# Kernel tuning notes

Hardware: AMD Instinct MI355X
Metric: run time of the kernel (lower is better)

The kernel has to match this reference:

```python
import jax, jax.numpy as jnp
import numpy as np

ALPHA = 0.2  # LeakyReLU negative slope

def setup_inputs() -> dict:
    key = jax.random.key(0)
    k1, k2 = jax.random.split(key)
    K, N = 4096, 1024
    x = jax.random.normal(k1, (K, N), dtype=jnp.float32)
    # xavier_uniform with gain 1.414 on shape (2N, 1)
    limit = 1.414 * np.sqrt(6.0 / (2 * N + 1))
    w = jax.random.uniform(k2, (2 * N, 1), dtype=jnp.float32, minval=-limit, maxval=limit)
    return {"x": x, "w": w}

def reference(x, w):
    # Faithful to: e[i,j] = leakyrelu(concat(x[i], x[j]) @ w)
    # Split w into halves -> outer-sum score (same math, no KxK x 2N intermediate).
    N = x.shape[1]
    w1 = w[:N, 0]   # (N,)
    w2 = w[N:, 0]   # (N,)
    s1 = x @ w1     # (K,)
    s2 = x @ w2     # (K,)
    e = jax.nn.leaky_relu(s1[:, None] + s2[None, :], negative_slope=ALPHA)  # (K, K)
    attention = jax.nn.softmax(e, axis=1)  # dropout p=0.0 -> identity
    h = attention @ x  # (K, N)
    return h
```

## Files before the change

kernel.cpp:

```cpp
#include <hip/hip_runtime.h>

#define KDIM 4096
#define NDIM 1024
#define ALPHA 0.2f
#define LOG2E 1.4426950408889634f
#define CCH 256
#define RCH 16
#define PFL 256

__device__ __align__(16) float g_s1L[KDIM];
__device__ __align__(16) float g_s2L[KDIM];
__device__ __align__(16) float g_E [2 * KDIM];
__device__ __align__(16) float g_F1[KDIM];
__device__ __align__(16) float g_F2[KDIM];
__device__ __align__(16) int   g_t  [KDIM];
__device__ __align__(16) int   g_sig[KDIM];
__device__ __align__(16) float g_cs [CCH][2 * NDIM];
__device__ __align__(16) float g_pre[CCH][2 * NDIM];
__device__ __align__(16) float g_tot[2 * NDIM];
__device__ __align__(16) float g_cz [2 * CCH];
__device__ __align__(16) float g_zpre[2 * CCH];
__device__ __align__(16) float g_ztot[2];

__global__ __launch_bounds__(256) void k_dots(const float* __restrict__ x,
                                              const float* __restrict__ w){
  const int wid = threadIdx.x >> 6, lane = threadIdx.x & 63;
  const int row = blockIdx.x * 4 + wid;
  const float* xr = x + (size_t)row * NDIM;
  float d1 = 0.f, d2 = 0.f;
  #pragma unroll
  for (int q = 0; q < 4; ++q){
    const int off = q * 256 + lane * 4;
    float4 X  = *(const float4*)(xr + off);
    float4 W1 = *(const float4*)(w + off);
    float4 W2 = *(const float4*)(w + NDIM + off);
    d1 = fmaf(X.x, W1.x, fmaf(X.y, W1.y, fmaf(X.z, W1.z, fmaf(X.w, W1.w, d1))));
    d2 = fmaf(X.x, W2.x, fmaf(X.y, W2.y, fmaf(X.z, W2.z, fmaf(X.w, W2.w, d2))));
  }
  #pragma unroll
  for (int m = 32; m >= 1; m >>= 1){
    d1 += __shfl_xor(d1, m, 64);
    d2 += __shfl_xor(d2, m, 64);
  }
  if (lane == 0){
    const float s1 = d1 * LOG2E, s2 = d2 * LOG2E;
    g_s1L[row] = s1;
    g_s2L[row] = s2;
    g_E[2 * row]     = __builtin_amdgcn_exp2f(s2);
    g_E[2 * row + 1] = __builtin_amdgcn_exp2f(ALPHA * s2);
    g_F1[row] = __builtin_amdgcn_exp2f(s1);
    g_F2[row] = __builtin_amdgcn_exp2f(ALPHA * s1);
  }
}

__global__ __launch_bounds__(256) void k_rank(){
  __shared__ __align__(16) float s2s[KDIM];
  const int tid = threadIdx.x;
  #pragma unroll
  for (int q = 0; q < 4; ++q)
    ((float4*)s2s)[q * 256 + tid] = ((const float4*)g_s2L)[q * 256 + tid];
  __syncthreads();
  const int grp = tid >> 4, sub = tid & 15;
  const int o = blockIdx.x * 16 + grp;
  int cnt = 0;
  if (o < KDIM){
    const float val = s2s[o];
    #pragma unroll 4
    for (int m = 0; m < 64; ++m){
      const int q4 = m * 16 + sub;
      const float4 v = ((const float4*)s2s)[q4];
      const int j0 = q4 * 4;
      cnt += (v.x > val || (v.x == val && (j0    ) < o));
      cnt += (v.y > val || (v.y == val && (j0 + 1) < o));
      cnt += (v.z > val || (v.z == val && (j0 + 2) < o));
      cnt += (v.w > val || (v.w == val && (j0 + 3) < o));
    }
  } else {
    const float thr = -g_s1L[o - KDIM];
    #pragma unroll 4
    for (int m = 0; m < 64; ++m){
      const int q4 = m * 16 + sub;
      const float4 v = ((const float4*)s2s)[q4];
      cnt += (v.x >= thr) + (v.y >= thr) + (v.z >= thr) + (v.w >= thr);
    }
  }
  cnt += __shfl_xor(cnt, 1, 64); cnt += __shfl_xor(cnt, 2, 64);
  cnt += __shfl_xor(cnt, 4, 64); cnt += __shfl_xor(cnt, 8, 64);
  if (sub == 0){
    if (o < KDIM) g_sig[cnt] = o;
    else          g_t[o - KDIM] = cnt;
  }
}

__global__ __launch_bounds__(256) void k_chunksum(const float* __restrict__ x){
  __shared__ int   js [RCH];
  __shared__ float e1s[RCH], e2s[RCH];
  const int c = blockIdx.x, tid = threadIdx.x;
  if (tid < RCH){
    const int j = g_sig[c * RCH + tid];
    js[tid]  = j;
    e1s[tid] = g_E[2 * j];
    e2s[tid] = g_E[2 * j + 1];
  }
  __syncthreads();
  if (tid == 0){
    float a = 0.f, b = 0.f;
    #pragma unroll
    for (int r = 0; r < RCH; ++r){ a += e1s[r]; b += e2s[r]; }
    g_cz[2 * c] = a; g_cz[2 * c + 1] = b;
  }
  float4 a1 = {0.f, 0.f, 0.f, 0.f}, a2 = {0.f, 0.f, 0.f, 0.f};
  #pragma unroll
  for (int r = 0; r < RCH; ++r){
    const float4 xv = *(const float4*)(x + (size_t)js[r] * NDIM + tid * 4);
    const float e1 = e1s[r], e2 = e2s[r];
    a1.x = fmaf(e1, xv.x, a1.x); a1.y = fmaf(e1, xv.y, a1.y);
    a1.z = fmaf(e1, xv.z, a1.z); a1.w = fmaf(e1, xv.w, a1.w);
    a2.x = fmaf(e2, xv.x, a2.x); a2.y = fmaf(e2, xv.y, a2.y);
    a2.z = fmaf(e2, xv.z, a2.z); a2.w = fmaf(e2, xv.w, a2.w);
  }
  *(float4*)&g_cs[c][tid * 4]        = a1;
  *(float4*)&g_cs[c][NDIM + tid * 4] = a2;
}

__global__ __launch_bounds__(256) void k_chunkscan(){
  __shared__ float TL[CCH][32];
  __shared__ float SS[8][32];
  const int tid = threadIdx.x;
  const int s = tid >> 5, k = tid & 31;
  const int col = blockIdx.x * 32 + k;
  float run = 0.f;
  #pragma unroll 8
  for (int m = 0; m < 32; ++m){
    const float v = g_cs[s * 32 + m][col];
    TL[s * 32 + m][k] = v;
    run += v;
  }
  SS[s][k] = run;
  __syncthreads();
  if (s == 0){
    float acc = 0.f;
    #pragma unroll
    for (int t = 0; t < 8; ++t){
      const float v = SS[t][k];
      SS[t][k] = acc;
      acc += v;
    }
    g_tot[col] = acc;
  }
  __syncthreads();
  run = SS[s][k];
  #pragma unroll 8
  for (int m = 0; m < 32; ++m){
    g_pre[s * 32 + m][col] = run;
    run += TL[s * 32 + m][k];
  }
  if (blockIdx.x == 0 && tid < 64){
    float v1[4], v2[4];
    #pragma unroll
    for (int q = 0; q < 4; ++q){
      v1[q] = g_cz[2 * (tid * 4 + q)];
      v2[q] = g_cz[2 * (tid * 4 + q) + 1];
    }
    const float s1 = v1[0] + v1[1] + v1[2] + v1[3];
    const float s2 = v2[0] + v2[1] + v2[2] + v2[3];
    float i1 = s1, i2 = s2;
    #pragma unroll
    for (int d = 1; d < 64; d <<= 1){
      const float t1 = __shfl_up(i1, d, 64);
      const float t2 = __shfl_up(i2, d, 64);
      if (tid >= d){ i1 += t1; i2 += t2; }
    }
    float e1 = i1 - s1, e2 = i2 - s2;
    #pragma unroll
    for (int q = 0; q < 4; ++q){
      g_zpre[2 * (tid * 4 + q)]     = e1;
      g_zpre[2 * (tid * 4 + q) + 1] = e2;
      e1 += v1[q]; e2 += v2[q];
    }
    if (tid == 63){ g_ztot[0] = e1; g_ztot[1] = e2; }
  }
}

__global__ __launch_bounds__(256) void k_emit(const float* __restrict__ x,
                                              float* __restrict__ out){
  __shared__ int    js [RCH];
  __shared__ float  e1s[RCH], e2s[RCH];
  __shared__ int    cnt[RCH + 1];
  __shared__ int    off[RCH + 2];
  __shared__ int    pos[RCH + 1];
  __shared__ int    ilist[KDIM];
  __shared__ float2 pfl[PFL];
  const int c = blockIdx.x, tid = threadIdx.x;
  const bool last = (c == CCH - 1);
  const int nbuck = last ? RCH + 1 : RCH;
  if (tid < RCH){
    const int j = g_sig[c * RCH + tid];
    js[tid]  = j;
    e1s[tid] = g_E[2 * j];
    e2s[tid] = g_E[2 * j + 1];
  }
  if (tid <= RCH) cnt[tid] = 0;
  __syncthreads();

  const int tbase = c * RCH;
  int myi[16], myr[16];
  #pragma unroll
  for (int q = 0; q < 16; ++q){
    const int i = q * 256 + tid;
    const int t = g_t[i];
    const int r = t - tbase;
    const bool in = (r >= 0) && (r < nbuck);
    myi[q] = i;
    myr[q] = in ? r : -1;
    if (in) atomicAdd(&cnt[r], 1);
  }
  __syncthreads();
  if (tid == 0){
    int run = 0;
    #pragma unroll
    for (int r = 0; r <= RCH; ++r){
      const int v = cnt[r];
      off[r] = run; pos[r] = run;
      run += v;
    }
    off[RCH + 1] = run;
  }
  __syncthreads();
  #pragma unroll
  for (int q = 0; q < 16; ++q){
    if (myr[q] >= 0){
      const int p = atomicAdd(&pos[myr[q]], 1);
      ilist[p] = myi[q];
      if (p < PFL)
        pfl[p] = make_float2(g_F1[myi[q]], g_F2[myi[q]]);
    }
  }
  __syncthreads();

  float4 a1 = *(const float4*)&g_pre[c][tid * 4];
  float4 a2 = *(const float4*)&g_pre[c][NDIM + tid * 4];
  const float4 t2 = *(const float4*)&g_tot[NDIM + tid * 4];
  float za1 = g_zpre[2 * c], za2 = g_zpre[2 * c + 1];
  const float zt2 = g_ztot[1];
  float4 v[RCH];
  #pragma unroll
  for (int r = 0; r < RCH; ++r)
    v[r] = *(const float4*)(x + (size_t)js[r] * NDIM + tid * 4);

  #pragma unroll
  for (int r = 0; r < RCH; ++r){
    for (int e = off[r]; e < off[r + 1]; ++e){
      const int i = ilist[e];
      float F1, F2;
      if (e < PFL){ const float2 pf = pfl[e]; F1 = pf.x; F2 = pf.y; }
      else        { F1 = g_F1[i]; F2 = g_F2[i]; }
      const float rz = 1.0f / fmaf(F1, za1, F2 * (zt2 - za2));
      float4 h;
      h.x = fmaf(F1, a1.x, F2 * (t2.x - a2.x)) * rz;
      h.y = fmaf(F1, a1.y, F2 * (t2.y - a2.y)) * rz;
      h.z = fmaf(F1, a1.z, F2 * (t2.z - a2.z)) * rz;
      h.w = fmaf(F1, a1.w, F2 * (t2.w - a2.w)) * rz;
      *(float4*)(out + (size_t)i * NDIM + tid * 4) = h;
    }
    const float e1 = e1s[r], e2 = e2s[r];
    za1 += e1; za2 += e2;
    const float4 xv = v[r];
    a1.x = fmaf(e1, xv.x, a1.x); a1.y = fmaf(e1, xv.y, a1.y);
    a1.z = fmaf(e1, xv.z, a1.z); a1.w = fmaf(e1, xv.w, a1.w);
    a2.x = fmaf(e2, xv.x, a2.x); a2.y = fmaf(e2, xv.y, a2.y);
    a2.z = fmaf(e2, xv.z, a2.z); a2.w = fmaf(e2, xv.w, a2.w);
  }
  if (last){
    for (int e = off[RCH]; e < off[RCH + 1]; ++e){
      const int i = ilist[e];
      float F1, F2;
      if (e < PFL){ const float2 pf = pfl[e]; F1 = pf.x; F2 = pf.y; }
      else        { F1 = g_F1[i]; F2 = g_F2[i]; }
      const float rz = 1.0f / fmaf(F1, za1, F2 * (zt2 - za2));
      float4 h;
      h.x = fmaf(F1, a1.x, F2 * (t2.x - a2.x)) * rz;
      h.y = fmaf(F1, a1.y, F2 * (t2.y - a2.y)) * rz;
      h.z = fmaf(F1, a1.z, F2 * (t2.z - a2.z)) * rz;
      h.w = fmaf(F1, a1.w, F2 * (t2.w - a2.w)) * rz;
      *(float4*)(out + (size_t)i * NDIM + tid * 4) = h;
    }
  }
}

extern "C" void kernel_launch(void* const* d_in, const int* in_sizes, int n_in,
                              void* d_out, int out_size, void* d_ws, size_t ws_size,
                              hipStream_t stream){
  const float* x = (const float*)d_in[0];
  const float* w = (const float*)d_in[1];
  float* out = (float*)d_out;
  (void)in_sizes; (void)n_in; (void)out_size; (void)d_ws; (void)ws_size;

  k_dots     <<<dim3(1024), dim3(256), 0, stream>>>(x, w);
  k_rank     <<<dim3(512),  dim3(256), 0, stream>>>();
  k_chunksum <<<dim3(CCH),  dim3(256), 0, stream>>>(x);
  k_chunkscan<<<dim3(64),   dim3(256), 0, stream>>>();
  k_emit     <<<dim3(CCH),  dim3(256), 0, stream>>>(x, out);
}
```

Measured before the change: 102.6 us.

## Fuse five-stage pipeline into one cooperative persistent kernel with grid syncs

Replaces the five separate launches (dots, rank, chunk sums, chunk scan, emit) with a single cooperative kernel of 256 blocks that moves between stages with grid.sync. Each chunk's x rows are held in registers from the chunk-sum stage and reused in the emit stage instead of being reloaded. The dot stage keeps w in registers and handles four rows per wave. The aim is to remove per-launch overhead and inter-kernel gaps. In exchange, the rank and dot stages now run on fewer blocks, and each grid barrier has its own cost. The old multi-launch path stays as a fallback if the cooperative launch fails.

After: 327.1 us. 219% more time.

```diff
diff --git a/kernel.cpp b/kernel.cpp
--- a/kernel.cpp
+++ b/kernel.cpp
@@ -1,4 +1,7 @@
 #include <hip/hip_runtime.h>
+#include <hip/hip_cooperative_groups.h>
+
+namespace cg = cooperative_groups;
 
 #define KDIM 4096
 #define NDIM 1024
@@ -21,6 +24,290 @@
 __device__ __align__(16) float g_cz [2 * CCH];
 __device__ __align__(16) float g_zpre[2 * CCH];
 __device__ __align__(16) float g_ztot[2];
+
+__global__ __launch_bounds__(256) void k_fused(const float* __restrict__ x,
+                                               const float* __restrict__ w,
+                                               float* __restrict__ out){
+  cg::grid_group grid = cg::this_grid();
+  __shared__ __align__(16) union {
+    float s2s[KDIM];
+    struct { float TL[CCH][32]; float SS[8][32]; } d;
+    struct {
+      int    js[RCH];
+      float  e1s[RCH], e2s[RCH];
+      int    cnt[RCH + 1], off[RCH + 2], pos[RCH + 1];
+      int    ilist[KDIM];
+      float2 pfl[PFL];
+    } e;
+  } sh;
+  const int tid = threadIdx.x, lane = tid & 63, wv = tid >> 6;
+  const int bid = blockIdx.x;
+
+  {
+    float4 W1r[4], W2r[4];
+    #pragma unroll
+    for (int q = 0; q < 4; ++q){
+      const int o = q * 256 + lane * 4;
+      W1r[q] = *(const float4*)(w + o);
+      W2r[q] = *(const float4*)(w + NDIM + o);
+    }
+    const int wgid = bid * 4 + wv;
+    #pragma unroll
+    for (int rr = 0; rr < 4; ++rr){
+      const int row = wgid * 4 + rr;
+      const float* xr = x + (size_t)row * NDIM;
+      float d1 = 0.f, d2 = 0.f;
+      #pragma unroll
+      for (int q = 0; q < 4; ++q){
+        const float4 X = *(const float4*)(xr + q * 256 + lane * 4);
+        d1 = fmaf(X.x, W1r[q].x, fmaf(X.y, W1r[q].y, fmaf(X.z, W1r[q].z, fmaf(X.w, W1r[q].w, d1))));
+        d2 = fmaf(X.x, W2r[q].x, fmaf(X.y, W2r[q].y, fmaf(X.z, W2r[q].z, fmaf(X.w, W2r[q].w, d2))));
+      }
+      #pragma unroll
+      for (int m = 32; m >= 1; m >>= 1){
+        d1 += __shfl_xor(d1, m, 64);
+        d2 += __shfl_xor(d2, m, 64);
+      }
+      if (lane == 0){
+        const float s1 = d1 * LOG2E, s2 = d2 * LOG2E;
+        g_s1L[row] = s1;
+        g_s2L[row] = s2;
+        g_E[2 * row]     = __builtin_amdgcn_exp2f(s2);
+        g_E[2 * row + 1] = __builtin_amdgcn_exp2f(ALPHA * s2);
+        g_F1[row] = __builtin_amdgcn_exp2f(s1);
+        g_F2[row] = __builtin_amdgcn_exp2f(ALPHA * s1);
+      }
+    }
+  }
+  __threadfence();
+  grid.sync();
+
+  {
+    #pragma unroll
+    for (int q = 0; q < 4; ++q)
+      ((float4*)sh.s2s)[q * 256 + tid] = ((const float4*)g_s2L)[q * 256 + tid];
+    __syncthreads();
+    const int grp = tid >> 4, sub = tid & 15;
+    #pragma unroll
+    for (int pass = 0; pass < 2; ++pass){
+      const int o = bid * 32 + pass * 16 + grp;
+      int cnt = 0;
+      if (o < KDIM){
+        const float val = sh.s2s[o];
+        #pragma unroll 4
+        for (int m = 0; m < 64; ++m){
+          const int q4 = m * 16 + sub;
+          const float4 v4 = ((const float4*)sh.s2s)[q4];
+          const int j0 = q4 * 4;
+          cnt += (v4.x > val || (v4.x == val && (j0    ) < o));
+          cnt += (v4.y > val || (v4.y == val && (j0 + 1) < o));
+          cnt += (v4.z > val || (v4.z == val && (j0 + 2) < o));
+          cnt += (v4.w > val || (v4.w == val && (j0 + 3) < o));
+        }
+      } else {
+        const float thr = -g_s1L[o - KDIM];
+        #pragma unroll 4
+        for (int m = 0; m < 64; ++m){
+          const int q4 = m * 16 + sub;
+          const float4 v4 = ((const float4*)sh.s2s)[q4];
+          cnt += (v4.x >= thr) + (v4.y >= thr) + (v4.z >= thr) + (v4.w >= thr);
+        }
+      }
+      cnt += __shfl_xor(cnt, 1, 64); cnt += __shfl_xor(cnt, 2, 64);
+      cnt += __shfl_xor(cnt, 4, 64); cnt += __shfl_xor(cnt, 8, 64);
+      if (sub == 0){
+        if (o < KDIM) g_sig[cnt] = o;
+        else          g_t[o - KDIM] = cnt;
+      }
+    }
+  }
+  __threadfence();
+  grid.sync();
+
+  float4 v[RCH];
+  {
+    const int c = bid;
+    if (tid < RCH){
+      const int j = g_sig[c * RCH + tid];
+      sh.e.js[tid]  = j;
+      sh.e.e1s[tid] = g_E[2 * j];
+      sh.e.e2s[tid] = g_E[2 * j + 1];
+    }
+    __syncthreads();
+    if (tid == 0){
+      float a = 0.f, b = 0.f;
+      #pragma unroll
+      for (int r = 0; r < RCH; ++r){ a += sh.e.e1s[r]; b += sh.e.e2s[r]; }
+      g_cz[2 * c] = a; g_cz[2 * c + 1] = b;
+    }
+    #pragma unroll
+    for (int r = 0; r < RCH; ++r)
+      v[r] = *(const float4*)(x + (size_t)sh.e.js[r] * NDIM + tid * 4);
+    float4 a1 = {0.f,0.f,0.f,0.f}, a2 = {0.f,0.f,0.f,0.f};
+    #pragma unroll
+    for (int r = 0; r < RCH; ++r){
+      const float e1 = sh.e.e1s[r], e2 = sh.e.e2s[r];
+      const float4 xv = v[r];
+      a1.x = fmaf(e1, xv.x, a1.x); a1.y = fmaf(e1, xv.y, a1.y);
+      a1.z = fmaf(e1, xv.z, a1.z); a1.w = fmaf(e1, xv.w, a1.w);
+      a2.x = fmaf(e2, xv.x, a2.x); a2.y = fmaf(e2, xv.y, a2.y);
+      a2.z = fmaf(e2, xv.z, a2.z); a2.w = fmaf(e2, xv.w, a2.w);
+    }
+    *(float4*)&g_cs[c][tid * 4]        = a1;
+    *(float4*)&g_cs[c][NDIM + tid * 4] = a2;
+  }
+  __threadfence();
+  grid.sync();
+
+  if (bid < 64){
+    const int s = tid >> 5, k2 = tid & 31;
+    const int col = bid * 32 + k2;
+    float run = 0.f;
+    #pragma unroll 8
+    for (int m = 0; m < 32; ++m){
+      const float vv = g_cs[s * 32 + m][col];
+      sh.d.TL[s * 32 + m][k2] = vv;
+      run += vv;
+    }
+    sh.d.SS[s][k2] = run;
+    __syncthreads();
+    if (s == 0){
+      float acc = 0.f;
+      #pragma unroll
+      for (int t = 0; t < 8; ++t){
+        const float vv = sh.d.SS[t][k2];
+        sh.d.SS[t][k2] = acc;
+        acc += vv;
+      }
+      g_tot[col] = acc;
+    }
+    __syncthreads();
+    run = sh.d.SS[s][k2];
+    #pragma unroll 8
+    for (int m = 0; m < 32; ++m){
+      g_pre[s * 32 + m][col] = run;
+      run += sh.d.TL[s * 32 + m][k2];
+    }
+  } else if (bid == 64 && tid < 64){
+    float v1[4], v2[4];
+    #pragma unroll
+    for (int q = 0; q < 4; ++q){
+      v1[q] = g_cz[2 * (tid * 4 + q)];
+      v2[q] = g_cz[2 * (tid * 4 + q) + 1];
+    }
+    const float s1 = v1[0] + v1[1] + v1[2] + v1[3];
+    const float s2 = v2[0] + v2[1] + v2[2] + v2[3];
+    float i1 = s1, i2 = s2;
+    #pragma unroll
+    for (int d = 1; d < 64; d <<= 1){
+      const float t1 = __shfl_up(i1, d, 64);
+      const float t2 = __shfl_up(i2, d, 64);
+      if (tid >= d){ i1 += t1; i2 += t2; }
+    }
+    float e1 = i1 - s1, e2 = i2 - s2;
+    #pragma unroll
+    for (int q = 0; q < 4; ++q){
+      g_zpre[2 * (tid * 4 + q)]     = e1;
+      g_zpre[2 * (tid * 4 + q) + 1] = e2;
+      e1 += v1[q]; e2 += v2[q];
+    }
+    if (tid == 63){ g_ztot[0] = e1; g_ztot[1] = e2; }
+  }
+  __threadfence();
+  grid.sync();
+
+  {
+    const int c = bid;
+    const bool last = (c == CCH - 1);
+    const int nbuck = last ? RCH + 1 : RCH;
+    if (tid < RCH){
+      const int j = g_sig[c * RCH + tid];
+      sh.e.js[tid]  = j;
+      sh.e.e1s[tid] = g_E[2 * j];
+      sh.e.e2s[tid] = g_E[2 * j + 1];
+    }
+    if (tid <= RCH) sh.e.cnt[tid] = 0;
+    __syncthreads();
+    const int tbase = c * RCH;
+    int myr[16];
+    #pragma unroll
+    for (int q = 0; q < 16; ++q){
+      const int i = q * 256 + tid;
+      const int t = g_t[i];
+      const int r = t - tbase;
+      const bool in = (r >= 0) && (r < nbuck);
+      myr[q] = in ? r : -1;
+      if (in) atomicAdd(&sh.e.cnt[r], 1);
+    }
+    __syncthreads();
+    if (tid == 0){
+      int run = 0;
+      #pragma unroll
+      for (int r = 0; r <= RCH; ++r){
+        const int vv = sh.e.cnt[r];
+        sh.e.off[r] = run; sh.e.pos[r] = run;
+        run += vv;
+      }
+      sh.e.off[RCH + 1] = run;
+    }
+    __syncthreads();
+    #pragma unroll
+    for (int q = 0; q < 16; ++q){
+      if (myr[q] >= 0){
+        const int i = q * 256 + tid;
+        const int p = atomicAdd(&sh.e.pos[myr[q]], 1);
+        sh.e.ilist[p] = i;
+        if (p < PFL) sh.e.pfl[p] = make_float2(g_F1[i], g_F2[i]);
+      }
+    }
+    __syncthreads();
+
+    float4 a1 = *(const float4*)&g_pre[c][tid * 4];
+    float4 a2 = *(const float4*)&g_pre[c][NDIM + tid * 4];
+    const float4 t2 = *(const float4*)&g_tot[NDIM + tid * 4];
+    float za1 = g_zpre[2 * c], za2 = g_zpre[2 * c + 1];
+    const float zt2 = g_ztot[1];
+
+    #pragma unroll
+    for (int r = 0; r < RCH; ++r){
+      for (int e = sh.e.off[r]; e < sh.e.off[r + 1]; ++e){
+        const int i = sh.e.ilist[e];
+        float F1, F2;
+        if (e < PFL){ const float2 pf = sh.e.pfl[e]; F1 = pf.x; F2 = pf.y; }
+        else        { F1 = g_F1[i]; F2 = g_F2[i]; }
+        const float rz = 1.0f / fmaf(F1, za1, F2 * (zt2 - za2));
+        float4 h;
+        h.x = fmaf(F1, a1.x, F2 * (t2.x - a2.x)) * rz;
+        h.y = fmaf(F1, a1.y, F2 * (t2.y - a2.y)) * rz;
+        h.z = fmaf(F1, a1.z, F2 * (t2.z - a2.z)) * rz;
+        h.w = fmaf(F1, a1.w, F2 * (t2.w - a2.w)) * rz;
+        *(float4*)(out + (size_t)i * NDIM + tid * 4) = h;
+      }
+      const float e1 = sh.e.e1s[r], e2 = sh.e.e2s[r];
+      za1 += e1; za2 += e2;
+      const float4 xv = v[r];
+      a1.x = fmaf(e1, xv.x, a1.x); a1.y = fmaf(e1, xv.y, a1.y);
+      a1.z = fmaf(e1, xv.z, a1.z); a1.w = fmaf(e1, xv.w, a1.w);
+      a2.x = fmaf(e2, xv.x, a2.x); a2.y = fmaf(e2, xv.y, a2.y);
+      a2.z = fmaf(e2, xv.z, a2.z); a2.w = fmaf(e2, xv.w, a2.w);
+    }
+    if (last){
+      for (int e = sh.e.off[RCH]; e < sh.e.off[RCH + 1]; ++e){
+        const int i = sh.e.ilist[e];
+        float F1, F2;
+        if (e < PFL){ const float2 pf = sh.e.pfl[e]; F1 = pf.x; F2 = pf.y; }
+        else        { F1 = g_F1[i]; F2 = g_F2[i]; }
+        const float rz = 1.0f / fmaf(F1, za1, F2 * (zt2 - za2));
+        float4 h;
+        h.x = fmaf(F1, a1.x, F2 * (t2.x - a2.x)) * rz;
+        h.y = fmaf(F1, a1.y, F2 * (t2.y - a2.y)) * rz;
+        h.z = fmaf(F1, a1.z, F2 * (t2.z - a2.z)) * rz;
+        h.w = fmaf(F1, a1.w, F2 * (t2.w - a2.w)) * rz;
+        *(float4*)(out + (size_t)i * NDIM + tid * 4) = h;
+      }
+    }
+  }
+}
 
 __global__ __launch_bounds__(256) void k_dots(const float* __restrict__ x,
                                               const float* __restrict__ w){
@@ -109,7 +396,7 @@
     for (int r = 0; r < RCH; ++r){ a += e1s[r]; b += e2s[r]; }
     g_cz[2 * c] = a; g_cz[2 * c + 1] = b;
   }
-  float4 a1 = {0.f, 0.f, 0.f, 0.f}, a2 = {0.f, 0.f, 0.f, 0.f};
+  float4 a1 = {0.f,0.f,0.f,0.f}, a2 = {0.f,0.f,0.f,0.f};
   #pragma unroll
   for (int r = 0; r < RCH; ++r){
     const float4 xv = *(const float4*)(x + (size_t)js[r] * NDIM + tid * 4);
@@ -202,16 +489,14 @@
   }
   if (tid <= RCH) cnt[tid] = 0;
   __syncthreads();
-
   const int tbase = c * RCH;
-  int myi[16], myr[16];
+  int myr[16];
   #pragma unroll
   for (int q = 0; q < 16; ++q){
     const int i = q * 256 + tid;
     const int t = g_t[i];
     const int r = t - tbase;
     const bool in = (r >= 0) && (r < nbuck);
-    myi[q] = i;
     myr[q] = in ? r : -1;
     if (in) atomicAdd(&cnt[r], 1);
   }
@@ -230,10 +515,10 @@
   #pragma unroll
   for (int q = 0; q < 16; ++q){
     if (myr[q] >= 0){
+      const int i = q * 256 + tid;
       const int p = atomicAdd(&pos[myr[q]], 1);
-      ilist[p] = myi[q];
-      if (p < PFL)
-        pfl[p] = make_float2(g_F1[myi[q]], g_F2[myi[q]]);
+      ilist[p] = i;
+      if (p < PFL) pfl[p] = make_float2(g_F1[i], g_F2[i]);
     }
   }
   __syncthreads();
@@ -296,9 +581,13 @@
   float* out = (float*)d_out;
   (void)in_sizes; (void)n_in; (void)out_size; (void)d_ws; (void)ws_size;
 
-  k_dots     <<<dim3(1024), dim3(256), 0, stream>>>(x, w);
-  k_rank     <<<dim3(512),  dim3(256), 0, stream>>>();
-  k_chunksum <<<dim3(CCH),  dim3(256), 0, stream>>>(x);
-  k_chunkscan<<<dim3(64),   dim3(256), 0, stream>>>();
-  k_emit     <<<dim3(CCH),  dim3(256), 0, stream>>>(x, out);
-}
+  void* args[] = { (void*)&x, (void*)&w, (void*)&out };
+  if (hipLaunchCooperativeKernel((const void*)k_fused, dim3(256), dim3(256),
+                                 args, 0, stream) != hipSuccess){
+    k_dots     <<<dim3(1024), dim3(256), 0, stream>>>(x, w);
+    k_rank     <<<dim3(512),  dim3(256), 0, stream>>>();
+    k_chunksum <<<dim3(CCH),  dim3(256), 0, stream>>>(x);
+    k_chunkscan<<<dim3(64),   dim3(256), 0, stream>>>();
+    k_emit     <<<dim3(CCH),  dim3(256), 0, stream>>>(x, out);
+  }
+}
```

## Fuse chunk-sum, scan and emit into one column-partitioned scan-emit kernel

Applied to the files above, without the earlier changes.

Replaces the three-kernel chunk-sum / chunk-scan / emit pipeline with a single kernel. Each block owns four output columns and scans over all 4096 sorted rows, using an in-block wave-shuffle prefix scan instead of global partial-sum buffers. It also bucket-sorts all rows by threshold in shared memory and packs F1/F2 into interleaved pairs. This removes two launches and the g_cs/g_pre round trips through global memory. The cost is that every block reads all of g_sig, g_t and g_E, gathers x with only 16-byte column slices per row, and writes output in scattered 16-byte pieces at one block per CU.

New measurement: 116.6 us. +13.6%, slower.

```diff
diff --git a/kernel.cpp b/kernel.cpp
--- a/kernel.cpp
+++ b/kernel.cpp
@@ -4,23 +4,13 @@
 #define NDIM 1024
 #define ALPHA 0.2f
 #define LOG2E 1.4426950408889634f
-#define CCH 256
-#define RCH 16
-#define PFL 256
 
 __device__ __align__(16) float g_s1L[KDIM];
 __device__ __align__(16) float g_s2L[KDIM];
 __device__ __align__(16) float g_E [2 * KDIM];
-__device__ __align__(16) float g_F1[KDIM];
-__device__ __align__(16) float g_F2[KDIM];
+__device__ __align__(16) float g_F [2 * KDIM];
 __device__ __align__(16) int   g_t  [KDIM];
 __device__ __align__(16) int   g_sig[KDIM];
-__device__ __align__(16) float g_cs [CCH][2 * NDIM];
-__device__ __align__(16) float g_pre[CCH][2 * NDIM];
-__device__ __align__(16) float g_tot[2 * NDIM];
-__device__ __align__(16) float g_cz [2 * CCH];
-__device__ __align__(16) float g_zpre[2 * CCH];
-__device__ __align__(16) float g_ztot[2];
 
 __global__ __launch_bounds__(256) void k_dots(const float* __restrict__ x,
                                               const float* __restrict__ w){
@@ -48,8 +38,8 @@
     g_s2L[row] = s2;
     g_E[2 * row]     = __builtin_amdgcn_exp2f(s2);
     g_E[2 * row + 1] = __builtin_amdgcn_exp2f(ALPHA * s2);
-    g_F1[row] = __builtin_amdgcn_exp2f(s1);
-    g_F2[row] = __builtin_amdgcn_exp2f(ALPHA * s1);
+    g_F[2 * row]     = __builtin_amdgcn_exp2f(s1);
+    g_F[2 * row + 1] = __builtin_amdgcn_exp2f(ALPHA * s1);
   }
 }
 
@@ -92,199 +82,149 @@
   }
 }
 
-__global__ __launch_bounds__(256) void k_chunksum(const float* __restrict__ x){
-  __shared__ int   js [RCH];
-  __shared__ float e1s[RCH], e2s[RCH];
-  const int c = blockIdx.x, tid = threadIdx.x;
-  if (tid < RCH){
-    const int j = g_sig[c * RCH + tid];
-    js[tid]  = j;
-    e1s[tid] = g_E[2 * j];
-    e2s[tid] = g_E[2 * j + 1];
-  }
-  __syncthreads();
-  if (tid == 0){
-    float a = 0.f, b = 0.f;
+__global__ __launch_bounds__(256, 1) void k_scanemit(const float* __restrict__ x,
+                                                     float* __restrict__ out){
+  __shared__ int   off [KDIM + 2];
+  __shared__ int   pos [KDIM + 1];
+  __shared__ int   ilist[KDIM];
+  __shared__ float wscan[4][10];
+  __shared__ int   iws[4];
+  const int tid = threadIdx.x, lane = tid & 63, wv = tid >> 6;
+  const int cg = ((blockIdx.x & 7) << 5) + (blockIdx.x >> 3);
+  const int c0 = cg * 4;
+
+  for (int b = tid; b < KDIM + 2; b += 256) off[b] = 0;
+
+  int js[16];
+  #pragma unroll
+  for (int q = 0; q < 4; ++q){
+    const int4 j4 = ((const int4*)g_sig)[tid * 4 + q];
+    js[q*4+0] = j4.x; js[q*4+1] = j4.y; js[q*4+2] = j4.z; js[q*4+3] = j4.w;
+  }
+  float e1[16], e2[16];
+  #pragma unroll
+  for (int r = 0; r < 16; ++r){
+    const float2 e = *(const float2*)&g_E[2 * js[r]];
+    e1[r] = e.x; e2[r] = e.y;
+  }
+  float4 v[16];
+  #pragma unroll
+  for (int r = 0; r < 16; ++r)
+    v[r] = *(const float4*)(x + (size_t)js[r] * NDIM + c0);
+
+  int tv[16];
+  #pragma unroll
+  for (int q = 0; q < 4; ++q){
+    const int4 t4 = ((const int4*)g_t)[tid * 4 + q];
+    tv[q*4+0] = t4.x; tv[q*4+1] = t4.y; tv[q*4+2] = t4.z; tv[q*4+3] = t4.w;
+  }
+  __syncthreads();
+  #pragma unroll
+  for (int r = 0; r < 16; ++r) atomicAdd(&off[tv[r]], 1);
+  __syncthreads();
+
+  int loc[16], myc = 0;
+  #pragma unroll
+  for (int r = 0; r < 16; ++r){ loc[r] = off[tid * 16 + r]; myc += loc[r]; }
+  int inc = myc;
+  #pragma unroll
+  for (int d = 1; d < 64; d <<= 1){
+    const int tmp = __shfl_up(inc, d, 64);
+    if (lane >= d) inc += tmp;
+  }
+  if (lane == 63) iws[wv] = inc;
+  __syncthreads();
+  int wpre = 0;
+  #pragma unroll
+  for (int w2 = 0; w2 < 4; ++w2) if (w2 < wv) wpre += iws[w2];
+  int run = wpre + inc - myc;
+  #pragma unroll
+  for (int r = 0; r < 16; ++r){ const int cc = loc[r]; off[tid * 16 + r] = run; run += cc; }
+  if (tid == 255){ off[KDIM] = run; off[KDIM + 1] = KDIM; }
+  __syncthreads();
+  for (int b = tid; b < KDIM + 1; b += 256) pos[b] = off[b];
+  __syncthreads();
+  #pragma unroll
+  for (int r = 0; r < 16; ++r){
+    const int p = atomicAdd(&pos[tv[r]], 1);
+    ilist[p] = tid * 16 + r;
+  }
+
+  float s[10] = {0,0,0,0,0,0,0,0,0,0};
+  #pragma unroll
+  for (int r = 0; r < 16; ++r){
+    s[0] = fmaf(e1[r], v[r].x, s[0]); s[1] = fmaf(e1[r], v[r].y, s[1]);
+    s[2] = fmaf(e1[r], v[r].z, s[2]); s[3] = fmaf(e1[r], v[r].w, s[3]);
+    s[4] = fmaf(e2[r], v[r].x, s[4]); s[5] = fmaf(e2[r], v[r].y, s[5]);
+    s[6] = fmaf(e2[r], v[r].z, s[6]); s[7] = fmaf(e2[r], v[r].w, s[7]);
+    s[8] += e1[r]; s[9] += e2[r];
+  }
+  float a[10];
+  #pragma unroll
+  for (int k = 0; k < 10; ++k) a[k] = s[k];
+  #pragma unroll
+  for (int d = 1; d < 64; d <<= 1){
+    float tmp[10];
     #pragma unroll
-    for (int r = 0; r < RCH; ++r){ a += e1s[r]; b += e2s[r]; }
-    g_cz[2 * c] = a; g_cz[2 * c + 1] = b;
-  }
-  float4 a1 = {0.f, 0.f, 0.f, 0.f}, a2 = {0.f, 0.f, 0.f, 0.f};
-  #pragma unroll
-  for (int r = 0; r < RCH; ++r){
-    const float4 xv = *(const float4*)(x + (size_t)js[r] * NDIM + tid * 4);
-    const float e1 = e1s[r], e2 = e2s[r];
-    a1.x = fmaf(e1, xv.x, a1.x); a1.y = fmaf(e1, xv.y, a1.y);
-    a1.z = fmaf(e1, xv.z, a1.z); a1.w = fmaf(e1, xv.w, a1.w);
-    a2.x = fmaf(e2, xv.x, a2.x); a2.y = fmaf(e2, xv.y, a2.y);
-    a2.z = fmaf(e2, xv.z, a2.z); a2.w = fmaf(e2, xv.w, a2.w);
-  }
-  *(float4*)&g_cs[c][tid * 4]        = a1;
-  *(float4*)&g_cs[c][NDIM + tid * 4] = a2;
-}
-
-__global__ __launch_bounds__(256) void k_chunkscan(){
-  __shared__ float TL[CCH][32];
-  __shared__ float SS[8][32];
-  const int tid = threadIdx.x;
-  const int s = tid >> 5, k = tid & 31;
-  const int col = blockIdx.x * 32 + k;
-  float run = 0.f;
-  #pragma unroll 8
-  for (int m = 0; m < 32; ++m){
-    const float v = g_cs[s * 32 + m][col];
-    TL[s * 32 + m][k] = v;
-    run += v;
-  }
-  SS[s][k] = run;
-  __syncthreads();
-  if (s == 0){
-    float acc = 0.f;
+    for (int k = 0; k < 10; ++k) tmp[k] = __shfl_up(a[k], d, 64);
+    if (lane >= d){
+      #pragma unroll
+      for (int k = 0; k < 10; ++k) a[k] += tmp[k];
+    }
+  }
+  if (lane == 63){
     #pragma unroll
-    for (int t = 0; t < 8; ++t){
-      const float v = SS[t][k];
-      SS[t][k] = acc;
-      acc += v;
-    }
-    g_tot[col] = acc;
-  }
-  __syncthreads();
-  run = SS[s][k];
-  #pragma unroll 8
-  for (int m = 0; m < 32; ++m){
-    g_pre[s * 32 + m][col] = run;
-    run += TL[s * 32 + m][k];
-  }
-  if (blockIdx.x == 0 && tid < 64){
-    float v1[4], v2[4];
+    for (int k = 0; k < 10; ++k) wscan[wv][k] = a[k];
+  }
+  __syncthreads();
+  float ex[10], tot[10];
+  #pragma unroll
+  for (int k = 0; k < 10; ++k){
+    float wp = 0.f, tt = 0.f;
     #pragma unroll
-    for (int q = 0; q < 4; ++q){
-      v1[q] = g_cz[2 * (tid * 4 + q)];
-      v2[q] = g_cz[2 * (tid * 4 + q) + 1];
-    }
-    const float s1 = v1[0] + v1[1] + v1[2] + v1[3];
-    const float s2 = v2[0] + v2[1] + v2[2] + v2[3];
-    float i1 = s1, i2 = s2;
-    #pragma unroll
-    for (int d = 1; d < 64; d <<= 1){
-      const float t1 = __shfl_up(i1, d, 64);
-      const float t2 = __shfl_up(i2, d, 64);
-      if (tid >= d){ i1 += t1; i2 += t2; }
-    }
-    float e1 = i1 - s1, e2 = i2 - s2;
-    #pragma unroll
-    for (int q = 0; q < 4; ++q){
-      g_zpre[2 * (tid * 4 + q)]     = e1;
-      g_zpre[2 * (tid * 4 + q) + 1] = e2;
-      e1 += v1[q]; e2 += v2[q];
-    }
-    if (tid == 63){ g_ztot[0] = e1; g_ztot[1] = e2; }
-  }
-}
-
-__global__ __launch_bounds__(256) void k_emit(const float* __restrict__ x,
-                                              float* __restrict__ out){
-  __shared__ int    js [RCH];
-  __shared__ float  e1s[RCH], e2s[RCH];
-  __shared__ int    cnt[RCH + 1];
-  __shared__ int    off[RCH + 2];
-  __shared__ int    pos[RCH + 1];
-  __shared__ int    ilist[KDIM];
-  __shared__ float2 pfl[PFL];
-  const int c = blockIdx.x, tid = threadIdx.x;
-  const bool last = (c == CCH - 1);
-  const int nbuck = last ? RCH + 1 : RCH;
-  if (tid < RCH){
-    const int j = g_sig[c * RCH + tid];
-    js[tid]  = j;
-    e1s[tid] = g_E[2 * j];
-    e2s[tid] = g_E[2 * j + 1];
-  }
-  if (tid <= RCH) cnt[tid] = 0;
-  __syncthreads();
-
-  const int tbase = c * RCH;
-  int myi[16], myr[16];
-  #pragma unroll
-  for (int q = 0; q < 16; ++q){
-    const int i = q * 256 + tid;
-    const int t = g_t[i];
-    const int r = t - tbase;
-    const bool in = (r >= 0) && (r < nbuck);
-    myi[q] = i;
-    myr[q] = in ? r : -1;
-    if (in) atomicAdd(&cnt[r], 1);
-  }
-  __syncthreads();
-  if (tid == 0){
-    int run = 0;
-    #pragma unroll
-    for (int r = 0; r <= RCH; ++r){
-      const int v = cnt[r];
-      off[r] = run; pos[r] = run;
-      run += v;
-    }
-    off[RCH + 1] = run;
-  }
-  __syncthreads();
-  #pragma unroll
-  for (int q = 0; q < 16; ++q){
-    if (myr[q] >= 0){
-      const int p = atomicAdd(&pos[myr[q]], 1);
-      ilist[p] = myi[q];
-      if (p < PFL)
-        pfl[p] = make_float2(g_F1[myi[q]], g_F2[myi[q]]);
-    }
-  }
-  __syncthreads();
-
-  float4 a1 = *(const float4*)&g_pre[c][tid * 4];
-  float4 a2 = *(const float4*)&g_pre[c][NDIM + tid * 4];
-  const float4 t2 = *(const float4*)&g_tot[NDIM + tid * 4];
-  float za1 = g_zpre[2 * c], za2 = g_zpre[2 * c + 1];
-  const float zt2 = g_ztot[1];
-  float4 v[RCH];
-  #pragma unroll
-  for (int r = 0; r < RCH; ++r)
-    v[r] = *(const float4*)(x + (size_t)js[r] * NDIM + tid * 4);
-
-  #pragma unroll
-  for (int r = 0; r < RCH; ++r){
-    for (int e = off[r]; e < off[r + 1]; ++e){
+    for (int w2 = 0; w2 < 4; ++w2){
+      const float vv = wscan[w2][k];
+      tt += vv;
+      if (w2 < wv) wp += vv;
+    }
+    ex[k]  = wp + a[k] - s[k];
+    tot[k] = tt;
+  }
+  float4 a1 = make_float4(ex[0], ex[1], ex[2], ex[3]);
+  float4 a2 = make_float4(ex[4], ex[5], ex[6], ex[7]);
+  float za1 = ex[8], za2 = ex[9];
+  const float4 t1 = make_float4(tot[0], tot[1], tot[2], tot[3]);
+  const float4 t2 = make_float4(tot[4], tot[5], tot[6], tot[7]);
+  const float zt1 = tot[8], zt2 = tot[9];
+
+  #pragma unroll
+  for (int r = 0; r < 16; ++r){
+    const int p = tid * 16 + r;
+    for (int e = off[p]; e < off[p + 1]; ++e){
       const int i = ilist[e];
-      float F1, F2;
-      if (e < PFL){ const float2 pf = pfl[e]; F1 = pf.x; F2 = pf.y; }
-      else        { F1 = g_F1[i]; F2 = g_F2[i]; }
+      const float2 Fp = *(const float2*)&g_F[2 * i];
+      const float F1 = Fp.x, F2 = Fp.y;
       const float rz = 1.0f / fmaf(F1, za1, F2 * (zt2 - za2));
       float4 h;
       h.x = fmaf(F1, a1.x, F2 * (t2.x - a2.x)) * rz;
       h.y = fmaf(F1, a1.y, F2 * (t2.y - a2.y)) * rz;
       h.z = fmaf(F1, a1.z, F2 * (t2.z - a2.z)) * rz;
       h.w = fmaf(F1, a1.w, F2 * (t2.w - a2.w)) * rz;
-      *(float4*)(out + (size_t)i * NDIM + tid * 4) = h;
-    }
-    const float e1 = e1s[r], e2 = e2s[r];
-    za1 += e1; za2 += e2;
-    const float4 xv = v[r];
-    a1.x = fmaf(e1, xv.x, a1.x); a1.y = fmaf(e1, xv.y, a1.y);
-    a1.z = fmaf(e1, xv.z, a1.z); a1.w = fmaf(e1, xv.w, a1.w);
-    a2.x = fmaf(e2, xv.x, a2.x); a2.y = fmaf(e2, xv.y, a2.y);
-    a2.z = fmaf(e2, xv.z, a2.z); a2.w = fmaf(e2, xv.w, a2.w);
-  }
-  if (last){
-    for (int e = off[RCH]; e < off[RCH + 1]; ++e){
-      const int i = ilist[e];
-      float F1, F2;
-      if (e < PFL){ const float2 pf = pfl[e]; F1 = pf.x; F2 = pf.y; }
-      else        { F1 = g_F1[i]; F2 = g_F2[i]; }
-      const float rz = 1.0f / fmaf(F1, za1, F2 * (zt2 - za2));
-      float4 h;
-      h.x = fmaf(F1, a1.x, F2 * (t2.x - a2.x)) * rz;
-      h.y = fmaf(F1, a1.y, F2 * (t2.y - a2.y)) * rz;
-      h.z = fmaf(F1, a1.z, F2 * (t2.z - a2.z)) * rz;
-      h.w = fmaf(F1, a1.w, F2 * (t2.w - a2.w)) * rz;
-      *(float4*)(out + (size_t)i * NDIM + tid * 4) = h;
-    }
+      *(float4*)(out + (size_t)i * NDIM + c0) = h;
+    }
+    za1 += e1[r]; za2 += e2[r];
+    a1.x = fmaf(e1[r], v[r].x, a1.x); a1.y = fmaf(e1[r], v[r].y, a1.y);
+    a1.z = fmaf(e1[r], v[r].z, a1.z); a1.w = fmaf(e1[r], v[r].w, a1.w);
+    a2.x = fmaf(e2[r], v[r].x, a2.x); a2.y = fmaf(e2[r], v[r].y, a2.y);
+    a2.z = fmaf(e2[r], v[r].z, a2.z); a2.w = fmaf(e2[r], v[r].w, a2.w);
+  }
+
+  const float rzz = 1.0f / zt1;
+  for (int e = off[KDIM] + tid; e < KDIM; e += 256){
+    const int i = ilist[e];
+    float4 h;
+    h.x = t1.x * rzz; h.y = t1.y * rzz; h.z = t1.z * rzz; h.w = t1.w * rzz;
+    *(float4*)(out + (size_t)i * NDIM + c0) = h;
   }
 }
 
@@ -296,9 +236,7 @@
   float* out = (float*)d_out;
   (void)in_sizes; (void)n_in; (void)out_size; (void)d_ws; (void)ws_size;
 
-  k_dots     <<<dim3(1024), dim3(256), 0, stream>>>(x, w);
-  k_rank     <<<dim3(512),  dim3(256), 0, stream>>>();
-  k_chunksum <<<dim3(CCH),  dim3(256), 0, stream>>>(x);
-  k_chunkscan<<<dim3(64),   dim3(256), 0, stream>>>();
-  k_emit     <<<dim3(CCH),  dim3(256), 0, stream>>>(x, out);
-}
+  k_dots    <<<dim3(1024), dim3(256), 0, stream>>>(x, w);
+  k_rank    <<<dim3(512),  dim3(256), 0, stream>>>();
+  k_scanemit<<<dim3(256),  dim3(256), 0, stream>>>(x, out);
+}
```
